# Kernel optimization log

Measured on AMD Instinct MI355X. Metric: run time of the kernel, lower is better.

Reference implementation:

```python
import jax, jax.numpy as jnp
import numpy as np

D_K = 64
NEG_INF = -1.0e9

def setup_inputs() -> dict:
    key = jax.random.key(0)
    kq, kk, kv, km = jax.random.split(key, 4)
    B, H, S, D = 2, 16, 2048, D_K
    Q = jax.random.normal(kq, (B, H, S, D), dtype=jnp.float32)
    K = jax.random.normal(kk, (B, H, S, D), dtype=jnp.float32)
    V = jax.random.normal(kv, (B, H, S, D), dtype=jnp.float32)
    # True entries are masked out (torch masked_fill semantics)
    attn_mask = jax.random.randint(km, (B, H, S, S), 0, 2).astype(jnp.bool_)
    return {"Q": Q, "K": K, "V": V, "attn_mask": attn_mask}

def reference(Q, K, V, attn_mask):
    # scores: [B, H, len_q, len_k]
    scale = 1.0 / np.sqrt(D_K).astype(np.float32)
    scores = jnp.einsum('bhqd,bhkd->bhqk', Q, K) * scale
    scores = jnp.where(attn_mask, jnp.float32(NEG_INF), scores)
    attn = jax.nn.softmax(scores, axis=-1)
    prob = jnp.einsum('bhqk,bhkd->bhqd', attn, V)
    return (prob, attn)
```

## Files before the change

### kernel.cpp

```cpp
#include <hip/hip_runtime.h>
#include <hip/hip_bf16.h>

#define S_LEN 2048
#define D_DIM 64
#define QT    64
#define KT    64
#define NTHR  256
#define NKT   (S_LEN / KT)
#define NBLK  1024
#define PROB_ELEMS 4194304LL

typedef float        f32x4  __attribute__((ext_vector_type(4)));
typedef int          i32x4  __attribute__((ext_vector_type(4)));
typedef unsigned int u32x4  __attribute__((ext_vector_type(4)));
typedef short        bf16x8 __attribute__((ext_vector_type(8)));

__device__ __forceinline__ unsigned short f2bf(float f) {
    return __builtin_bit_cast(unsigned short, __float2bfloat16(f));
}
__device__ __forceinline__ int swzc(int row, int ch) {
    return ch ^ ((row ^ (row >> 3)) & 7);
}
__device__ __forceinline__ float4 scale4(float4 v, float s) {
    v.x *= s; v.y *= s; v.z *= s; v.w *= s; return v;
}
__device__ __forceinline__ u32x4 packbf(float4 a, float4 b) {
    u32x4 r;
    r[0] = (unsigned)f2bf(a.x) | ((unsigned)f2bf(a.y) << 16);
    r[1] = (unsigned)f2bf(a.z) | ((unsigned)f2bf(a.w) << 16);
    r[2] = (unsigned)f2bf(b.x) | ((unsigned)f2bf(b.y) << 16);
    r[3] = (unsigned)f2bf(b.z) | ((unsigned)f2bf(b.w) << 16);
    return r;
}
__device__ __forceinline__ unsigned cvtpk(float lo, float hi) {
    unsigned r;
    asm("v_cvt_pk_bf16_f32 %0, %1, %2" : "=v"(r) : "v"(lo), "v"(hi));
    return r;
}
__device__ __forceinline__ void glds16(const unsigned* g, unsigned char* l) {
    __builtin_amdgcn_global_load_lds(
        (const __attribute__((address_space(1))) unsigned*)g,
        (__attribute__((address_space(3))) unsigned*)(void*)l, 16, 0, 0);
}

__global__ void mask_probe_kernel(const unsigned int* __restrict__ m,
                                  int* __restrict__ flag) {
    unsigned int v = m[threadIdx.x];
    unsigned long long ok = __ballot(v <= 1u);
    if (threadIdx.x == 0) *flag = (ok == ~0ULL) ? 1 : 0;
}

#define KPART 524288
#define VPART 65536
__global__ __launch_bounds__(256)
void kv_prep(const float* __restrict__ Kg, const float* __restrict__ Vg,
             unsigned* __restrict__ Kbf, unsigned* __restrict__ Vtb) {
    int tid = blockIdx.x * 256 + threadIdx.x;
    if (tid < KPART) {
        int ch = tid & 7, rowg = tid >> 3;
        const float* src = Kg + (long long)rowg * D_DIM + ch * 8;
        float4 a = *(const float4*)src, b = *(const float4*)(src + 4);
        int bh = rowg >> 11, k = rowg & 2047, kt = k >> 6, row = k & 63;
        unsigned* dst = Kbf + ((unsigned)(bh * NKT + kt) << 11)
                            + row * 32 + swzc(row, ch) * 4;
        *(u32x4*)dst = packbf(a, b);
    } else if (tid < KPART + VPART) {
        int idx = tid - KPART;
        int d = idx & 63, kt = (idx >> 6) & 31, bh = idx >> 11;
        const float* vb = Vg + (long long)(bh * S_LEN + kt * KT) * D_DIM + d;
        unsigned* tile = Vtb + ((unsigned)(bh * NKT + kt) << 11) + d * 32;
        #pragma unroll
        for (int ci = 0; ci < 8; ++ci) {
            u32x4 o;
            #pragma unroll
            for (int s = 0; s < 4; ++s) {
                float lo = vb[(ci * 8 + 2 * s) * D_DIM];
                float hi = vb[(ci * 8 + 2 * s + 1) * D_DIM];
                o[s] = (unsigned)f2bf(lo) | ((unsigned)f2bf(hi) << 16);
            }
            *(u32x4*)(tile + swzc(d, ci) * 4) = o;
        }
    }
}


#define LOAD_MBITS(DST, KTV)                                                \
    { unsigned bz = 0u;                                                     \
      _Pragma("unroll")                                                     \
      for (int n = 0; n < 4; ++n) {                                         \
        unsigned idx = rowoff + (unsigned)((KTV) * KT + n * 16 + 4 * g);    \
        if (mask32) {                                                       \
            i32x4 m4 = *(const i32x4*)(((const int*)maskB) + idx);          \
            bz |= ((m4[0] ? 1u : 0u) | (m4[1] ? 2u : 0u) |                  \
                   (m4[2] ? 4u : 0u) | (m4[3] ? 8u : 0u)) << (n * 4);       \
        } else {                                                            \
            unsigned mb = *(const unsigned*)(maskB + idx);                  \
            bz |= (((mb & 0xffu) ? 1u : 0u) | ((mb & 0xff00u) ? 2u : 0u) |  \
                   ((mb & 0xff0000u) ? 4u : 0u) |                           \
                   ((mb & 0xff000000u) ? 8u : 0u)) << (n * 4);              \
        } }                                                                 \
      (DST) = bz; }

#define LOAD_BITS2(DST, KTV)                                                \
    { if (useWS) (DST) = (unsigned)bitsWS[bitbase + (unsigned)(KTV) * NTHR];\
      else LOAD_MBITS(DST, KTV) }

#define PH1_TILE(KS, BITS)                                                  \
    { unsigned bb = (BITS);                                                 \
      _Pragma("unroll")                                                     \
      for (int n = 0; n < 4; ++n) {                                         \
        int rowk = n * 16 + c;                                              \
        bf16x8 kf0 = *(const bf16x8*)((KS) + rowk * 128 + swzc(rowk, g) * 16);     \
        bf16x8 kf1 = *(const bf16x8*)((KS) + rowk * 128 + swzc(rowk, 4 + g) * 16); \
        f32x4 acc = {0.f, 0.f, 0.f, 0.f};                                   \
        acc = __builtin_amdgcn_mfma_f32_16x16x32_bf16(kf0, qf0, acc, 0, 0, 0); \
        acc = __builtin_amdgcn_mfma_f32_16x16x32_bf16(kf1, qf1, acc, 0, 0, 0); \
        unsigned mb = bb >> (n * 4);                                        \
        psum += (mb & 1u) ? 0.f : __expf(acc[0]);                           \
        psum += (mb & 2u) ? 0.f : __expf(acc[1]);                           \
        psum += (mb & 4u) ? 0.f : __expf(acc[2]);                           \
        psum += (mb & 8u) ? 0.f : __expf(acc[3]);                           \
      } }

#define PH2_TILE(KS, VT, BITS, KTV)                                         \
    { unsigned bb = (BITS);                                                 \
      _Pragma("unroll")                                                     \
      for (int n = 0; n < 4; ++n) {                                         \
        int rowk = n * 16 + c;                                              \
        bf16x8 kf0 = *(const bf16x8*)((KS) + rowk * 128 + swzc(rowk, g) * 16);     \
        bf16x8 kf1 = *(const bf16x8*)((KS) + rowk * 128 + swzc(rowk, 4 + g) * 16); \
        f32x4 acc = {0.f, 0.f, 0.f, 0.f};                                   \
        acc = __builtin_amdgcn_mfma_f32_16x16x32_bf16(kf0, qf0, acc, 0, 0, 0); \
        acc = __builtin_amdgcn_mfma_f32_16x16x32_bf16(kf1, qf1, acc, 0, 0, 0); \
        unsigned mb = bb >> (n * 4);                                        \
        f32x4 ev;                                                           \
        ev[0] = (mb & 1u) ? 0.f : __expf(acc[0]) * rinv;                    \
        ev[1] = (mb & 2u) ? 0.f : __expf(acc[1]) * rinv;                    \
        ev[2] = (mb & 4u) ? 0.f : __expf(acc[2]) * rinv;                    \
        ev[3] = (mb & 8u) ? 0.f : __expf(acc[3]) * rinv;                    \
        unsigned idx0 = rowoff + (unsigned)((KTV) * KT + n * 16 + 4 * g);   \
        __builtin_nontemporal_store(ev, (f32x4*)(attnOut + idx0));          \
        uint2 pkv; pkv.x = cvtpk(ev[0], ev[1]); pkv.y = cvtpk(ev[2], ev[3]);\
        int kloc = n * 16 + 4 * g;                                          \
        *(uint2*)(Ps + ql * 128 + swzc(ql, kloc >> 3) * 16 + (kloc & 7) * 2) = pkv; \
      }                                                                     \
      { bf16x8 pa0 = *(const bf16x8*)(Ps + ql * 128 + swzc(ql, g) * 16);    \
        bf16x8 pa1 = *(const bf16x8*)(Ps + ql * 128 + swzc(ql, 4 + g) * 16);\
        __builtin_amdgcn_s_setprio(1);                                      \
        _Pragma("unroll")                                                   \
        for (int df = 0; df < 4; ++df) {                                    \
            int d = df * 16 + c;                                            \
            bf16x8 vb0 = *(const bf16x8*)((VT) + d * 128 + swzc(d, g) * 16);     \
            bf16x8 vb1 = *(const bf16x8*)((VT) + d * 128 + swzc(d, 4 + g) * 16); \
            pacc[df] = __builtin_amdgcn_mfma_f32_16x16x32_bf16(pa0, vb0, pacc[df], 0, 0, 0); \
            pacc[df] = __builtin_amdgcn_mfma_f32_16x16x32_bf16(pa1, vb1, pacc[df], 0, 0, 0); \
        }                                                                   \
        __builtin_amdgcn_s_setprio(0); } }

__global__ __launch_bounds__(NTHR, 4)
void attn_fused_glds(const float* __restrict__ Qg,
                     const unsigned* __restrict__ Kbf,
                     const unsigned* __restrict__ Vtb,
                     const unsigned char* __restrict__ maskB,
                     const int* __restrict__ flagp,
                     unsigned short* __restrict__ bitsWS, int useWS,
                     float* __restrict__ attnOut, float* __restrict__ probOut) {
    __shared__ unsigned char sm[40960];
    unsigned char* Ks0 = sm;
    unsigned char* Ks1 = sm + 8192;
    unsigned char* Vt0 = sm + 16384;
    unsigned char* Vt1 = sm + 24576;
    unsigned char* Ps  = sm + 32768;

    const int t = threadIdx.x;
    const int lane = t & 63, w = t >> 6, c = lane & 15, g = lane >> 4;

    const int orig = blockIdx.x;
    const int virt = (orig & 7) * 128 + (orig >> 3);
    const int qt = virt & 31, bh = virt >> 5;
    const int mask32 = *flagp;

    const int qrowbase = bh * S_LEN + qt * QT;
    const int ql = w * 16 + c;
    const unsigned rowoff = (unsigned)(qrowbase + ql) * (unsigned)S_LEN;
    const unsigned bitbase = (unsigned)virt * NKT * NTHR + (unsigned)t;
    const unsigned ktile0 = (unsigned)(bh * NKT) << 11;

    const int f0u = t * 4, f1u = (NTHR + t) * 4;
    const int dst0 = (t & ~63) * 16, dst1 = (NTHR + (t & ~63)) * 16;

    #pragma unroll
    for (int i = 0; i < 2; ++i) {
        int flat = i * NTHR + t, row = flat >> 3, ch = flat & 7;
        const float* src = Qg + (qrowbase + row) * D_DIM + ch * 8;
        float4 a = *(const float4*)src, b = *(const float4*)(src + 4);
        *(u32x4*)(Ps + row * 128 + swzc(row, ch) * 16) =
            packbf(scale4(a, 0.125f), scale4(b, 0.125f));
    }
    __syncthreads();
    bf16x8 qf0 = *(const bf16x8*)(Ps + ql * 128 + swzc(ql, g) * 16);
    bf16x8 qf1 = *(const bf16x8*)(Ps + ql * 128 + swzc(ql, 4 + g) * 16);

    float psum = 0.f;
    unsigned bA, bB;
    {
        const unsigned* kp = Kbf + ktile0;
        glds16(kp + f0u, Ks0 + dst0);
        glds16(kp + f1u, Ks0 + dst1);
    }
    LOAD_MBITS(bA, 0)

    for (int j = 0; j < NKT / 2; ++j) {
        const int ktA = 2 * j, ktB = 2 * j + 1;
        __syncthreads();
        {
            const unsigned* kp = Kbf + ktile0 + (unsigned)ktB * 2048;
            glds16(kp + f0u, Ks1 + dst0);
            glds16(kp + f1u, Ks1 + dst1);
        }
        LOAD_MBITS(bB, ktB)
        PH1_TILE(Ks0, bA)
        if (useWS) bitsWS[bitbase + (unsigned)ktA * NTHR] = (unsigned short)bA;

        __syncthreads();
        if (j + 1 < NKT / 2) {
            const unsigned* kp = Kbf + ktile0 + (unsigned)(ktA + 2) * 2048;
            glds16(kp + f0u, Ks0 + dst0);
            glds16(kp + f1u, Ks0 + dst1);
            LOAD_MBITS(bA, ktA + 2)
        }
        PH1_TILE(Ks1, bB)
        if (useWS) bitsWS[bitbase + (unsigned)ktB * NTHR] = (unsigned short)bB;
    }

    float s = psum;
    s += __shfl_xor(s, 16, 64);
    s += __shfl_xor(s, 32, 64);
    const float rinv = 1.0f / s;

    f32x4 pacc[4];
    #pragma unroll
    for (int d = 0; d < 4; ++d) pacc[d] = (f32x4){0.f, 0.f, 0.f, 0.f};

    {
        const unsigned* kp = Kbf + ktile0;
        const unsigned* vp = Vtb + ktile0;
        glds16(kp + f0u, Ks0 + dst0); glds16(kp + f1u, Ks0 + dst1);
        glds16(vp + f0u, Vt0 + dst0); glds16(vp + f1u, Vt0 + dst1);
    }
    LOAD_BITS2(bA, 0)

    for (int j = 0; j < NKT / 2; ++j) {
        const int ktA = 2 * j, ktB = 2 * j + 1;
        __syncthreads();
        {
            const unsigned* kp = Kbf + ktile0 + (unsigned)ktB * 2048;
            const unsigned* vp = Vtb + ktile0 + (unsigned)ktB * 2048;
            glds16(kp + f0u, Ks1 + dst0); glds16(kp + f1u, Ks1 + dst1);
            glds16(vp + f0u, Vt1 + dst0); glds16(vp + f1u, Vt1 + dst1);
        }
        LOAD_BITS2(bB, ktB)
        PH2_TILE(Ks0, Vt0, bA, ktA)

        __syncthreads();
        if (j + 1 < NKT / 2) {
            const unsigned* kp = Kbf + ktile0 + (unsigned)(ktA + 2) * 2048;
            const unsigned* vp = Vtb + ktile0 + (unsigned)(ktA + 2) * 2048;
            glds16(kp + f0u, Ks0 + dst0); glds16(kp + f1u, Ks0 + dst1);
            glds16(vp + f0u, Vt0 + dst0); glds16(vp + f1u, Vt0 + dst1);
            LOAD_BITS2(bA, ktA + 2)
        }
        PH2_TILE(Ks1, Vt1, bB, ktB)
    }

    #pragma unroll
    for (int df = 0; df < 4; ++df)
        #pragma unroll
        for (int r = 0; r < 4; ++r) {
            int qe = w * 16 + g * 4 + r;
            probOut[(long long)(qrowbase + qe) * D_DIM + df * 16 + c] = pacc[df][r];
        }
}

#define LOAD_K(KP, KTV)                                                     \
    { _Pragma("unroll")                                                     \
      for (int i = 0; i < 2; ++i) {                                         \
        int flat = i * NTHR + t, row = flat >> 3, ch = flat & 7;            \
        const float* src = Kg + (kbase + (KTV) * KT + row) * D_DIM + ch * 8;\
        float4 a = *(const float4*)src, b = *(const float4*)(src + 4);      \
        KP[i] = packbf(a, b);                                               \
      } }
#define STAGE_K(KS, KP)                                                     \
    { _Pragma("unroll")                                                     \
      for (int i = 0; i < 2; ++i) {                                         \
        int flat = i * NTHR + t, row = flat >> 3, ch = flat & 7;            \
        *(u32x4*)((KS) + row * 128 + swzc(row, ch) * 16) = KP[i];           \
      } }
#define LOAD_V(VP, KTV)                                                     \
    { const float* src = Vg + (kbase + (KTV) * KT + k0v) * D_DIM + dgv * 8; \
      float4 a = *(const float4*)src, b = *(const float4*)(src + 4);        \
      float4 e4 = *(const float4*)(src + D_DIM);                            \
      float4 f4 = *(const float4*)(src + D_DIM + 4);                        \
      VP[0] = (unsigned)f2bf(a.x) | ((unsigned)f2bf(e4.x) << 16);           \
      VP[1] = (unsigned)f2bf(a.y) | ((unsigned)f2bf(e4.y) << 16);           \
      VP[2] = (unsigned)f2bf(a.z) | ((unsigned)f2bf(e4.z) << 16);           \
      VP[3] = (unsigned)f2bf(a.w) | ((unsigned)f2bf(e4.w) << 16);           \
      VP[4] = (unsigned)f2bf(b.x) | ((unsigned)f2bf(f4.x) << 16);           \
      VP[5] = (unsigned)f2bf(b.y) | ((unsigned)f2bf(f4.y) << 16);           \
      VP[6] = (unsigned)f2bf(b.z) | ((unsigned)f2bf(f4.z) << 16);           \
      VP[7] = (unsigned)f2bf(b.w) | ((unsigned)f2bf(f4.w) << 16); }
#define STAGE_V(VT, VP)                                                     \
    { _Pragma("unroll")                                                     \
      for (int jj = 0; jj < 8; ++jj) {                                      \
        int d = dgv * 8 + jj;                                               \
        *(unsigned*)((VT) + d * 128 + swzc(d, k0v >> 3) * 16 + (k0v & 7) * 2) = VP[jj]; \
      } }

__global__ __launch_bounds__(NTHR, 4)
void attn_fused_reg(const float* __restrict__ Qg, const float* __restrict__ Kg,
                    const float* __restrict__ Vg,
                    const unsigned char* __restrict__ maskB,
                    const int* __restrict__ flagp,
                    unsigned short* __restrict__ bitsWS, int useWS,
                    float* __restrict__ attnOut, float* __restrict__ probOut) {
    __shared__ unsigned char sm[40960];
    unsigned char* Ks0 = sm;
    unsigned char* Ks1 = sm + 8192;
    unsigned char* Vt0 = sm + 16384;
    unsigned char* Vt1 = sm + 24576;
    unsigned char* Ps  = sm + 32768;

    const int t = threadIdx.x;
    const int lane = t & 63, w = t >> 6, c = lane & 15, g = lane >> 4;

    const int orig = blockIdx.x;
    const int virt = (orig & 7) * 128 + (orig >> 3);
    const int qt = virt & 31, bh = virt >> 5;
    const int mask32 = *flagp;

    const int qrowbase = bh * S_LEN + qt * QT;
    const int kbase = bh * S_LEN;
    const int ql = w * 16 + c;
    const unsigned rowoff = (unsigned)(qrowbase + ql) * (unsigned)S_LEN;
    const unsigned bitbase = (unsigned)virt * NKT * NTHR + (unsigned)t;
    const int dgv = t & 7, k0v = (t >> 3) * 2;

    #pragma unroll
    for (int i = 0; i < 2; ++i) {
        int flat = i * NTHR + t, row = flat >> 3, ch = flat & 7;
        const float* src = Qg + (qrowbase + row) * D_DIM + ch * 8;
        float4 a = *(const float4*)src, b = *(const float4*)(src + 4);
        *(u32x4*)(Ps + row * 128 + swzc(row, ch) * 16) =
            packbf(scale4(a, 0.125f), scale4(b, 0.125f));
    }
    __syncthreads();
    bf16x8 qf0 = *(const bf16x8*)(Ps + ql * 128 + swzc(ql, g) * 16);
    bf16x8 qf1 = *(const bf16x8*)(Ps + ql * 128 + swzc(ql, 4 + g) * 16);
    __syncthreads();

    float psum = 0.f;
    u32x4 kpA[2], kpB[2];
    unsigned bA, bB;
    LOAD_K(kpA, 0)
    LOAD_MBITS(bA, 0)

    for (int j = 0; j < NKT / 2; ++j) {
        const int ktA = 2 * j, ktB = 2 * j + 1;
        STAGE_K(Ks0, kpA)
        LOAD_K(kpB, ktB)
        LOAD_MBITS(bB, ktB)
        __syncthreads();
        PH1_TILE(Ks0, bA)
        if (useWS) bitsWS[bitbase + (unsigned)ktA * NTHR] = (unsigned short)bA;
        STAGE_K(Ks1, kpB)
        if (j + 1 < NKT / 2) {
            LOAD_K(kpA, ktA + 2)
            LOAD_MBITS(bA, ktA + 2)
        }
        __syncthreads();
        PH1_TILE(Ks1, bB)
        if (useWS) bitsWS[bitbase + (unsigned)ktB * NTHR] = (unsigned short)bB;
    }

    float s = psum;
    s += __shfl_xor(s, 16, 64);
    s += __shfl_xor(s, 32, 64);
    const float rinv = 1.0f / s;

    f32x4 pacc[4];
    #pragma unroll
    for (int d = 0; d < 4; ++d) pacc[d] = (f32x4){0.f, 0.f, 0.f, 0.f};

    unsigned vpA[8], vpB[8];
    LOAD_K(kpA, 0)
    LOAD_V(vpA, 0)
    LOAD_BITS2(bA, 0)
    __syncthreads();

    for (int j = 0; j < NKT / 2; ++j) {
        const int ktA = 2 * j, ktB = 2 * j + 1;
        STAGE_K(Ks0, kpA)
        STAGE_V(Vt0, vpA)
        LOAD_K(kpB, ktB)
        LOAD_V(vpB, ktB)
        LOAD_BITS2(bB, ktB)
        __syncthreads();
        PH2_TILE(Ks0, Vt0, bA, ktA)
        STAGE_K(Ks1, kpB)
        STAGE_V(Vt1, vpB)
        if (j + 1 < NKT / 2) {
            LOAD_K(kpA, ktA + 2)
            LOAD_V(vpA, ktA + 2)
            LOAD_BITS2(bA, ktA + 2)
        }
        __syncthreads();
        PH2_TILE(Ks1, Vt1, bB, ktB)
    }

    #pragma unroll
    for (int df = 0; df < 4; ++df)
        #pragma unroll
        for (int r = 0; r < 4; ++r) {
            int qe = w * 16 + g * 4 + r;
            probOut[(long long)(qrowbase + qe) * D_DIM + df * 16 + c] = pacc[df][r];
        }
}

extern "C" void kernel_launch(void* const* d_in, const int* in_sizes, int n_in,
                              void* d_out, int out_size, void* d_ws, size_t ws_size,
                              hipStream_t stream) {
    const float* Q = (const float*)d_in[0];
    const float* K = (const float*)d_in[1];
    const float* V = (const float*)d_in[2];
    const unsigned char* mask = (const unsigned char*)d_in[3];

    float* prob = (float*)d_out;
    float* attn = (float*)d_out + PROB_ELEMS;

    const size_t bits_bytes = (size_t)NBLK * NKT * NTHR * 2ull;
    const size_t kbf_bytes  = 8388608ull;
    int* flag = (int*)d_ws;
    unsigned short* bitsWS = (unsigned short*)((char*)d_ws + 256);
    unsigned* Kbf = (unsigned*)((char*)d_ws + 256 + bits_bytes);
    unsigned* Vtb = (unsigned*)((char*)d_ws + 256 + bits_bytes + kbf_bytes);

    const int useWS   = (ws_size >= 256 + bits_bytes) ? 1 : 0;
    const int usePrep = (ws_size >= 256 + bits_bytes + 2 * kbf_bytes) ? 1 : 0;

    mask_probe_kernel<<<1, 64, 0, stream>>>((const unsigned int*)mask, flag);
    if (usePrep) {
        kv_prep<<<(KPART + VPART) / 256, 256, 0, stream>>>(K, V, Kbf, Vtb);
        attn_fused_glds<<<NBLK, NTHR, 0, stream>>>(Q, Kbf, Vtb, mask, flag,
                                                   bitsWS, useWS, attn, prob);
    } else {
        attn_fused_reg<<<NBLK, NTHR, 0, stream>>>(Q, K, V, mask, flag,
                                                  bitsWS, useWS, attn, prob);
    }
}
```

Baseline: 365.3 us.

## Split key range across waves with MFMA-fragment K/V layout loaded directly to registers

Replaces the LDS-staged global_load_lds kernel with a new kernel that uses 32-row query tiles and splits each 64-key tile between two waves. K and V are pre-packed into per-lane MFMA fragment order, so each wave loads its operands straight from global memory into registers, with no LDS staging and no per-tile barriers. Row sums and the partial P·V accumulators are combined across the two wave halves through shared memory, and the mask bit cache shrinks to 8-bit entries. The block count doubles and occupancy is hinted at 4 blocks per CU. In exchange it adds a cross-wave reduction and relies on L2 to serve K/V reads that LDS used to share.

Measured after the change: 441.5 us. +20.9%, slower.

```diff
diff --git a/kernel.cpp b/kernel.cpp
--- a/kernel.cpp
+++ b/kernel.cpp
@@ -3,11 +3,12 @@
 
 #define S_LEN 2048
 #define D_DIM 64
-#define QT    64
+#define QT    32
 #define KT    64
 #define NTHR  256
 #define NKT   (S_LEN / KT)
-#define NBLK  1024
+#define NQT   (S_LEN / QT)
+#define NBLK  (NQT * 32)
 #define PROB_ELEMS 4194304LL
 
 typedef float        f32x4  __attribute__((ext_vector_type(4)));
@@ -37,11 +38,8 @@
     asm("v_cvt_pk_bf16_f32 %0, %1, %2" : "=v"(r) : "v"(lo), "v"(hi));
     return r;
 }
-__device__ __forceinline__ void glds16(const unsigned* g, unsigned char* l) {
-    __builtin_amdgcn_global_load_lds(
-        (const __attribute__((address_space(1))) unsigned*)g,
-        (__attribute__((address_space(3))) unsigned*)(void*)l, 16, 0, 0);
-}
+#define BC8(x) __builtin_bit_cast(bf16x8, (x))
+#define MFMA(A, B, C) __builtin_amdgcn_mfma_f32_16x16x32_bf16((A), (B), (C), 0, 0, 0)
 
 __global__ void mask_probe_kernel(const unsigned int* __restrict__ m,
                                   int* __restrict__ flag) {
@@ -50,59 +48,278 @@
     if (threadIdx.x == 0) *flag = (ok == ~0ULL) ? 1 : 0;
 }
 
-#define KPART 524288
-#define VPART 65536
+#define KFRAG_T 524288
+#define VFRAG_T 524288
 __global__ __launch_bounds__(256)
-void kv_prep(const float* __restrict__ Kg, const float* __restrict__ Vg,
-             unsigned* __restrict__ Kbf, unsigned* __restrict__ Vtb) {
+void kv_prep_split(const float* __restrict__ Kg, const float* __restrict__ Vg,
+                   unsigned* __restrict__ Kf, unsigned* __restrict__ Vf) {
     int tid = blockIdx.x * 256 + threadIdx.x;
-    if (tid < KPART) {
-        int ch = tid & 7, rowg = tid >> 3;
-        const float* src = Kg + (long long)rowg * D_DIM + ch * 8;
+    if (tid < KFRAG_T) {
+        int l = tid & 63, f = (tid >> 6) & 1, n = (tid >> 7) & 1;
+        int wk = (tid >> 8) & 1, kt = (tid >> 9) & 31, bh = tid >> 14;
+        int c = l & 15, g = l >> 4;
+        const float* src = Kg
+            + (long long)(bh * S_LEN + kt * KT + wk * 32 + n * 16 + c) * D_DIM
+            + f * 32 + g * 8;
         float4 a = *(const float4*)src, b = *(const float4*)(src + 4);
-        int bh = rowg >> 11, k = rowg & 2047, kt = k >> 6, row = k & 63;
-        unsigned* dst = Kbf + ((unsigned)(bh * NKT + kt) << 11)
-                            + row * 32 + swzc(row, ch) * 4;
+        unsigned* dst = Kf + ((unsigned)(bh * NKT + kt) << 11)
+                           + (unsigned)((wk * 4 + n * 2 + f) * 64 + l) * 4u;
         *(u32x4*)dst = packbf(a, b);
-    } else if (tid < KPART + VPART) {
-        int idx = tid - KPART;
-        int d = idx & 63, kt = (idx >> 6) & 31, bh = idx >> 11;
-        const float* vb = Vg + (long long)(bh * S_LEN + kt * KT) * D_DIM + d;
-        unsigned* tile = Vtb + ((unsigned)(bh * NKT + kt) << 11) + d * 32;
+    } else if (tid < KFRAG_T + VFRAG_T) {
+        int idx = tid - KFRAG_T;
+        int l = idx & 63, df = (idx >> 6) & 3;
+        int wk = (idx >> 8) & 1, kt = (idx >> 9) & 31, bh = idx >> 14;
+        int c = l & 15, g = l >> 4;
+        const float* vb = Vg
+            + (long long)(bh * S_LEN + kt * KT + wk * 32 + g * 8) * D_DIM
+            + df * 16 + c;
+        u32x4 o;
         #pragma unroll
-        for (int ci = 0; ci < 8; ++ci) {
-            u32x4 o;
+        for (int s = 0; s < 4; ++s) {
+            float lo = vb[(2 * s) * D_DIM];
+            float hi = vb[(2 * s + 1) * D_DIM];
+            o[s] = (unsigned)f2bf(lo) | ((unsigned)f2bf(hi) << 16);
+        }
+        unsigned* dst = Vf + ((unsigned)(bh * NKT + kt) << 11)
+                           + (unsigned)((wk * 4 + df) * 64 + l) * 4u;
+        *(u32x4*)dst = o;
+    }
+}
+
+#define LOAD_KF(DST, KTV)                                                   \
+    { const u32x4* p_ = (const u32x4*)(Kf + tbase + (unsigned)(KTV) * 2048u \
+                                       + (unsigned)wk * 1024u) + lane;      \
+      DST[0] = p_[0]; DST[1] = p_[64]; DST[2] = p_[128]; DST[3] = p_[192]; }
+
+#define LOAD_VF(DST, KTV)                                                   \
+    { const u32x4* p_ = (const u32x4*)(Vf + tbase + (unsigned)(KTV) * 2048u \
+                                       + (unsigned)wk * 1024u) + lane;      \
+      DST[0] = p_[0]; DST[1] = p_[64]; DST[2] = p_[128]; DST[3] = p_[192]; }
+
+#define PREF_MSK(M4, R2, KTV)                                               \
+    { if (mask32) {                                                         \
+        _Pragma("unroll")                                                   \
+        for (int n_ = 0; n_ < 2; ++n_)                                      \
+          M4[n_] = *(const i32x4*)(maskI + rowoff                           \
+                     + (unsigned)((KTV) * KT + wk * 32 + n_ * 16 + 4 * g)); \
+      } else {                                                              \
+        _Pragma("unroll")                                                   \
+        for (int n_ = 0; n_ < 2; ++n_)                                      \
+          R2[n_] = *(const unsigned*)(maskB + rowoff                        \
+                     + (unsigned)((KTV) * KT + wk * 32 + n_ * 16 + 4 * g)); \
+      } }
+
+#define BITS8(DST, M4, R2)                                                  \
+    { unsigned bz_ = 0u;                                                    \
+      if (mask32) {                                                         \
+        _Pragma("unroll")                                                   \
+        for (int n_ = 0; n_ < 2; ++n_)                                      \
+          bz_ |= ((M4[n_][0] ? 1u : 0u) | (M4[n_][1] ? 2u : 0u) |           \
+                  (M4[n_][2] ? 4u : 0u) | (M4[n_][3] ? 8u : 0u)) << (n_*4); \
+      } else {                                                              \
+        _Pragma("unroll")                                                   \
+        for (int n_ = 0; n_ < 2; ++n_) { unsigned mb_ = R2[n_];             \
+          bz_ |= (((mb_ & 0xffu) ? 1u : 0u) | ((mb_ & 0xff00u) ? 2u : 0u) | \
+                  ((mb_ & 0xff0000u) ? 4u : 0u) |                           \
+                  ((mb_ & 0xff000000u) ? 8u : 0u)) << (n_ * 4); }           \
+      }                                                                     \
+      (DST) = bz_; }
+
+#define LOAD_B8(DST, KTV)                                                   \
+    { if (useWS) (DST) = (unsigned)bitsWS[bitbase + (unsigned)(KTV)*NTHR];  \
+      else { i32x4 mq_[2]; unsigned rq_[2];                                 \
+             PREF_MSK(mq_, rq_, KTV) BITS8(DST, mq_, rq_) } }
+
+#define QK4(KC, A0, A1)                                                     \
+    { A0 = (f32x4){0.f,0.f,0.f,0.f}; A1 = (f32x4){0.f,0.f,0.f,0.f};         \
+      A0 = MFMA(BC8(KC[0]), qf0, A0); A0 = MFMA(BC8(KC[1]), qf1, A0);       \
+      A1 = MFMA(BC8(KC[2]), qf0, A1); A1 = MFMA(BC8(KC[3]), qf1, A1); }
+
+#define PH1(KC, BITS)                                                       \
+    { f32x4 a0_, a1_; QK4(KC, a0_, a1_)                                     \
+      unsigned bb_ = (BITS);                                                \
+      psum += (bb_ &   1u) ? 0.f : __expf(a0_[0]);                          \
+      psum += (bb_ &   2u) ? 0.f : __expf(a0_[1]);                          \
+      psum += (bb_ &   4u) ? 0.f : __expf(a0_[2]);                          \
+      psum += (bb_ &   8u) ? 0.f : __expf(a0_[3]);                          \
+      psum += (bb_ &  16u) ? 0.f : __expf(a1_[0]);                          \
+      psum += (bb_ &  32u) ? 0.f : __expf(a1_[1]);                          \
+      psum += (bb_ &  64u) ? 0.f : __expf(a1_[2]);                          \
+      psum += (bb_ & 128u) ? 0.f : __expf(a1_[3]); }
+
+#define PH2(KC, VC, BITS, KTV)                                              \
+    { f32x4 a0_, a1_; QK4(KC, a0_, a1_)                                     \
+      unsigned bb_ = (BITS);                                                \
+      f32x4 e0_, e1_;                                                       \
+      e0_[0] = (bb_ &   1u) ? 0.f : __expf(a0_[0]) * rinv;                  \
+      e0_[1] = (bb_ &   2u) ? 0.f : __expf(a0_[1]) * rinv;                  \
+      e0_[2] = (bb_ &   4u) ? 0.f : __expf(a0_[2]) * rinv;                  \
+      e0_[3] = (bb_ &   8u) ? 0.f : __expf(a0_[3]) * rinv;                  \
+      e1_[0] = (bb_ &  16u) ? 0.f : __expf(a1_[0]) * rinv;                  \
+      e1_[1] = (bb_ &  32u) ? 0.f : __expf(a1_[1]) * rinv;                  \
+      e1_[2] = (bb_ &  64u) ? 0.f : __expf(a1_[2]) * rinv;                  \
+      e1_[3] = (bb_ & 128u) ? 0.f : __expf(a1_[3]) * rinv;                  \
+      unsigned ix_ = rowoff + (unsigned)((KTV) * KT + wk * 32 + 4 * g);     \
+      *(f32x4*)(attnOut + ix_)      = e0_;                                  \
+      *(f32x4*)(attnOut + ix_ + 16) = e1_;                                  \
+      { uint2 p0_, p1_;                                                     \
+        p0_.x = cvtpk(e0_[0], e0_[1]); p0_.y = cvtpk(e0_[2], e0_[3]);       \
+        p1_.x = cvtpk(e1_[0], e1_[1]); p1_.y = cvtpk(e1_[2], e1_[3]);       \
+        *(uint2*)(PsW + c * 80 + 8 * g)      = p0_;                         \
+        *(uint2*)(PsW + c * 80 + 32 + 8 * g) = p1_; }                       \
+      { bf16x8 pa_ = *(const bf16x8*)(PsW + c * 80 + 16 * g);               \
+        __builtin_amdgcn_s_setprio(1);                                      \
+        pacc[0] = MFMA(pa_, BC8(VC[0]), pacc[0]);                           \
+        pacc[1] = MFMA(pa_, BC8(VC[1]), pacc[1]);                           \
+        pacc[2] = MFMA(pa_, BC8(VC[2]), pacc[2]);                           \
+        pacc[3] = MFMA(pa_, BC8(VC[3]), pacc[3]);                           \
+        __builtin_amdgcn_s_setprio(0); } }
+
+#define QS_OFF 0
+#define PS_OFF 4096
+#define RS_OFF 9216
+#define SMB    9472
+
+__global__ __launch_bounds__(NTHR, 4)
+void attn_fused_split(const float* __restrict__ Qg,
+                      const unsigned* __restrict__ Kf,
+                      const unsigned* __restrict__ Vf,
+                      const unsigned char* __restrict__ maskB,
+                      const int* __restrict__ flagp,
+                      unsigned char* __restrict__ bitsWS, int useWS,
+                      float* __restrict__ attnOut, float* __restrict__ probOut) {
+    __shared__ unsigned char sm[SMB];
+
+    const int t = threadIdx.x;
+    const int lane = t & 63, w = t >> 6, c = lane & 15, g = lane >> 4;
+    const int wq = w >> 1, wk = w & 1;
+
+    const int orig = blockIdx.x;
+    const int virt = (orig & 7) * 256 + (orig >> 3);
+    const int qt = virt & (NQT - 1), bh = virt >> 6;
+    const int mask32 = *flagp;
+    const int* maskI = (const int*)maskB;
+
+    const int qrowbase = bh * S_LEN + qt * QT;
+    const unsigned rowoff = (unsigned)(qrowbase + wq * 16 + c) * (unsigned)S_LEN;
+    const unsigned bitbase = (unsigned)virt * NKT * NTHR + (unsigned)t;
+    const unsigned tbase = (unsigned)(bh * NKT) << 11;
+    unsigned char* PsW = sm + PS_OFF + w * 1280;
+
+    {
+        int row = t >> 3, ch = t & 7;
+        const float* src = Qg + (qrowbase + row) * D_DIM + ch * 8;
+        float4 a = *(const float4*)src, b = *(const float4*)(src + 4);
+        *(u32x4*)(sm + QS_OFF + row * 128 + swzc(row, ch) * 16) =
+            packbf(scale4(a, 0.125f), scale4(b, 0.125f));
+    }
+    __syncthreads();
+    bf16x8 qf0, qf1;
+    {
+        int row = wq * 16 + c;
+        qf0 = *(const bf16x8*)(sm + QS_OFF + row * 128 + swzc(row, g) * 16);
+        qf1 = *(const bf16x8*)(sm + QS_OFF + row * 128 + swzc(row, 4 + g) * 16);
+    }
+
+    float psum = 0.f;
+    {
+        u32x4 kA[4], kB[4];
+        i32x4 mA[2], mB[2];
+        unsigned rA[2], rB[2], bA, bB;
+        LOAD_KF(kA, 0)
+        PREF_MSK(mA, rA, 0)
+        for (int j = 0; j < NKT / 2; ++j) {
+            const int ktA = 2 * j, ktB = 2 * j + 1;
+            LOAD_KF(kB, ktB)
+            PREF_MSK(mB, rB, ktB)
+            BITS8(bA, mA, rA)
+            PH1(kA, bA)
+            if (useWS) bitsWS[bitbase + (unsigned)ktA * NTHR] = (unsigned char)bA;
+            if (j + 1 < NKT / 2) {
+                LOAD_KF(kA, ktA + 2)
+                PREF_MSK(mA, rA, ktA + 2)
+            }
+            BITS8(bB, mB, rB)
+            PH1(kB, bB)
+            if (useWS) bitsWS[bitbase + (unsigned)ktB * NTHR] = (unsigned char)bB;
+        }
+    }
+    {
+        float s = psum;
+        s += __shfl_xor(s, 16, 64);
+        s += __shfl_xor(s, 32, 64);
+        float* Rs = (float*)(sm + RS_OFF);
+        if (lane < 16) Rs[w * 16 + c] = s;
+    }
+    __syncthreads();
+    const float rinv = 1.0f /
+        (((const float*)(sm + RS_OFF))[(wq * 2 + 0) * 16 + c] +
+         ((const float*)(sm + RS_OFF))[(wq * 2 + 1) * 16 + c]);
+
+    f32x4 pacc[4];
+    #pragma unroll
+    for (int d = 0; d < 4; ++d) pacc[d] = (f32x4){0.f, 0.f, 0.f, 0.f};
+    {
+        u32x4 kA[4], kB[4], vA[4], vB[4];
+        unsigned bA, bB;
+        LOAD_KF(kA, 0)
+        LOAD_B8(bA, 0)
+        for (int j = 0; j < NKT / 2; ++j) {
+            const int ktA = 2 * j, ktB = 2 * j + 1;
+            LOAD_KF(kB, ktB)
+            LOAD_B8(bB, ktB)
+            LOAD_VF(vA, ktA)
+            PH2(kA, vA, bA, ktA)
+            if (j + 1 < NKT / 2) {
+                LOAD_KF(kA, ktA + 2)
+                LOAD_B8(bA, ktA + 2)
+            }
+            LOAD_VF(vB, ktB)
+            PH2(kB, vB, bB, ktB)
+        }
+    }
+
+    __syncthreads();
+    if (wk == 1) {
+        #pragma unroll
+        for (int df = 0; df < 4; ++df)
+            *(f32x4*)(sm + wq * 4096 + lane * 64 + df * 16) = pacc[df];
+    }
+    __syncthreads();
+    if (wk == 0) {
+        #pragma unroll
+        for (int df = 0; df < 4; ++df) {
+            f32x4 o = pacc[df] +
+                *(const f32x4*)(sm + wq * 4096 + lane * 64 + df * 16);
             #pragma unroll
-            for (int s = 0; s < 4; ++s) {
-                float lo = vb[(ci * 8 + 2 * s) * D_DIM];
-                float hi = vb[(ci * 8 + 2 * s + 1) * D_DIM];
-                o[s] = (unsigned)f2bf(lo) | ((unsigned)f2bf(hi) << 16);
+            for (int r = 0; r < 4; ++r) {
+                int qe = qrowbase + wq * 16 + 4 * g + r;
+                probOut[(long long)qe * D_DIM + df * 16 + c] = o[r];
             }
-            *(u32x4*)(tile + swzc(d, ci) * 4) = o;
-        }
-    }
-}
-
-
+        }
+    }
+}
+
+#define FKT 64
 #define LOAD_MBITS(DST, KTV)                                                \
-    { unsigned bz = 0u;                                                     \
+    { unsigned bz_ = 0u;                                                    \
       _Pragma("unroll")                                                     \
-      for (int n = 0; n < 4; ++n) {                                         \
-        unsigned idx = rowoff + (unsigned)((KTV) * KT + n * 16 + 4 * g);    \
+      for (int n_ = 0; n_ < 4; ++n_) {                                      \
+        unsigned idx_ = rowoff + (unsigned)((KTV) * FKT + n_ * 16 + 4 * g); \
         if (mask32) {                                                       \
-            i32x4 m4 = *(const i32x4*)(((const int*)maskB) + idx);          \
-            bz |= ((m4[0] ? 1u : 0u) | (m4[1] ? 2u : 0u) |                  \
-                   (m4[2] ? 4u : 0u) | (m4[3] ? 8u : 0u)) << (n * 4);       \
+            i32x4 m4_ = *(const i32x4*)(maskI + idx_);                      \
+            bz_ |= ((m4_[0] ? 1u : 0u) | (m4_[1] ? 2u : 0u) |               \
+                    (m4_[2] ? 4u : 0u) | (m4_[3] ? 8u : 0u)) << (n_ * 4);   \
         } else {                                                            \
-            unsigned mb = *(const unsigned*)(maskB + idx);                  \
-            bz |= (((mb & 0xffu) ? 1u : 0u) | ((mb & 0xff00u) ? 2u : 0u) |  \
-                   ((mb & 0xff0000u) ? 4u : 0u) |                           \
-                   ((mb & 0xff000000u) ? 8u : 0u)) << (n * 4);              \
+            unsigned mb_ = *(const unsigned*)(maskB + idx_);                \
+            bz_ |= (((mb_ & 0xffu) ? 1u : 0u) | ((mb_ & 0xff00u) ? 2u : 0u) | \
+                    ((mb_ & 0xff0000u) ? 4u : 0u) |                         \
+                    ((mb_ & 0xff000000u) ? 8u : 0u)) << (n_ * 4);           \
         } }                                                                 \
-      (DST) = bz; }
+      (DST) = bz_; }
 
 #define LOAD_BITS2(DST, KTV)                                                \
-    { if (useWS) (DST) = (unsigned)bitsWS[bitbase + (unsigned)(KTV) * NTHR];\
+    { if (useWS) (DST) = (unsigned)bitsW16[bitbase + (unsigned)(KTV)*NTHR]; \
       else LOAD_MBITS(DST, KTV) }
 
 #define PH1_TILE(KS, BITS)                                                  \
@@ -113,8 +330,7 @@
         bf16x8 kf0 = *(const bf16x8*)((KS) + rowk * 128 + swzc(rowk, g) * 16);     \
         bf16x8 kf1 = *(const bf16x8*)((KS) + rowk * 128 + swzc(rowk, 4 + g) * 16); \
         f32x4 acc = {0.f, 0.f, 0.f, 0.f};                                   \
-        acc = __builtin_amdgcn_mfma_f32_16x16x32_bf16(kf0, qf0, acc, 0, 0, 0); \
-        acc = __builtin_amdgcn_mfma_f32_16x16x32_bf16(kf1, qf1, acc, 0, 0, 0); \
+        acc = MFMA(kf0, qf0, acc); acc = MFMA(kf1, qf1, acc);               \
         unsigned mb = bb >> (n * 4);                                        \
         psum += (mb & 1u) ? 0.f : __expf(acc[0]);                           \
         psum += (mb & 2u) ? 0.f : __expf(acc[1]);                           \
@@ -130,163 +346,35 @@
         bf16x8 kf0 = *(const bf16x8*)((KS) + rowk * 128 + swzc(rowk, g) * 16);     \
         bf16x8 kf1 = *(const bf16x8*)((KS) + rowk * 128 + swzc(rowk, 4 + g) * 16); \
         f32x4 acc = {0.f, 0.f, 0.f, 0.f};                                   \
-        acc = __builtin_amdgcn_mfma_f32_16x16x32_bf16(kf0, qf0, acc, 0, 0, 0); \
-        acc = __builtin_amdgcn_mfma_f32_16x16x32_bf16(kf1, qf1, acc, 0, 0, 0); \
+        acc = MFMA(kf0, qf0, acc); acc = MFMA(kf1, qf1, acc);               \
         unsigned mb = bb >> (n * 4);                                        \
         f32x4 ev;                                                           \
         ev[0] = (mb & 1u) ? 0.f : __expf(acc[0]) * rinv;                    \
         ev[1] = (mb & 2u) ? 0.f : __expf(acc[1]) * rinv;                    \
         ev[2] = (mb & 4u) ? 0.f : __expf(acc[2]) * rinv;                    \
         ev[3] = (mb & 8u) ? 0.f : __expf(acc[3]) * rinv;                    \
-        unsigned idx0 = rowoff + (unsigned)((KTV) * KT + n * 16 + 4 * g);   \
-        __builtin_nontemporal_store(ev, (f32x4*)(attnOut + idx0));          \
+        unsigned idx0 = rowoff + (unsigned)((KTV) * FKT + n * 16 + 4 * g);  \
+        *(f32x4*)(attnOut + idx0) = ev;                                     \
         uint2 pkv; pkv.x = cvtpk(ev[0], ev[1]); pkv.y = cvtpk(ev[2], ev[3]);\
         int kloc = n * 16 + 4 * g;                                          \
         *(uint2*)(Ps + ql * 128 + swzc(ql, kloc >> 3) * 16 + (kloc & 7) * 2) = pkv; \
       }                                                                     \
       { bf16x8 pa0 = *(const bf16x8*)(Ps + ql * 128 + swzc(ql, g) * 16);    \
         bf16x8 pa1 = *(const bf16x8*)(Ps + ql * 128 + swzc(ql, 4 + g) * 16);\
-        __builtin_amdgcn_s_setprio(1);                                      \
         _Pragma("unroll")                                                   \
         for (int df = 0; df < 4; ++df) {                                    \
             int d = df * 16 + c;                                            \
             bf16x8 vb0 = *(const bf16x8*)((VT) + d * 128 + swzc(d, g) * 16);     \
             bf16x8 vb1 = *(const bf16x8*)((VT) + d * 128 + swzc(d, 4 + g) * 16); \
-            pacc[df] = __builtin_amdgcn_mfma_f32_16x16x32_bf16(pa0, vb0, pacc[df], 0, 0, 0); \
-            pacc[df] = __builtin_amdgcn_mfma_f32_16x16x32_bf16(pa1, vb1, pacc[df], 0, 0, 0); \
-        }                                                                   \
-        __builtin_amdgcn_s_setprio(0); } }
-
-__global__ __launch_bounds__(NTHR, 4)
-void attn_fused_glds(const float* __restrict__ Qg,
-                     const unsigned* __restrict__ Kbf,
-                     const unsigned* __restrict__ Vtb,
-                     const unsigned char* __restrict__ maskB,
-                     const int* __restrict__ flagp,
-                     unsigned short* __restrict__ bitsWS, int useWS,
-                     float* __restrict__ attnOut, float* __restrict__ probOut) {
-    __shared__ unsigned char sm[40960];
-    unsigned char* Ks0 = sm;
-    unsigned char* Ks1 = sm + 8192;
-    unsigned char* Vt0 = sm + 16384;
-    unsigned char* Vt1 = sm + 24576;
-    unsigned char* Ps  = sm + 32768;
-
-    const int t = threadIdx.x;
-    const int lane = t & 63, w = t >> 6, c = lane & 15, g = lane >> 4;
-
-    const int orig = blockIdx.x;
-    const int virt = (orig & 7) * 128 + (orig >> 3);
-    const int qt = virt & 31, bh = virt >> 5;
-    const int mask32 = *flagp;
-
-    const int qrowbase = bh * S_LEN + qt * QT;
-    const int ql = w * 16 + c;
-    const unsigned rowoff = (unsigned)(qrowbase + ql) * (unsigned)S_LEN;
-    const unsigned bitbase = (unsigned)virt * NKT * NTHR + (unsigned)t;
-    const unsigned ktile0 = (unsigned)(bh * NKT) << 11;
-
-    const int f0u = t * 4, f1u = (NTHR + t) * 4;
-    const int dst0 = (t & ~63) * 16, dst1 = (NTHR + (t & ~63)) * 16;
-
-    #pragma unroll
-    for (int i = 0; i < 2; ++i) {
-        int flat = i * NTHR + t, row = flat >> 3, ch = flat & 7;
-        const float* src = Qg + (qrowbase + row) * D_DIM + ch * 8;
-        float4 a = *(const float4*)src, b = *(const float4*)(src + 4);
-        *(u32x4*)(Ps + row * 128 + swzc(row, ch) * 16) =
-            packbf(scale4(a, 0.125f), scale4(b, 0.125f));
-    }
-    __syncthreads();
-    bf16x8 qf0 = *(const bf16x8*)(Ps + ql * 128 + swzc(ql, g) * 16);
-    bf16x8 qf1 = *(const bf16x8*)(Ps + ql * 128 + swzc(ql, 4 + g) * 16);
-
-    float psum = 0.f;
-    unsigned bA, bB;
-    {
-        const unsigned* kp = Kbf + ktile0;
-        glds16(kp + f0u, Ks0 + dst0);
-        glds16(kp + f1u, Ks0 + dst1);
-    }
-    LOAD_MBITS(bA, 0)
-
-    for (int j = 0; j < NKT / 2; ++j) {
-        const int ktA = 2 * j, ktB = 2 * j + 1;
-        __syncthreads();
-        {
-            const unsigned* kp = Kbf + ktile0 + (unsigned)ktB * 2048;
-            glds16(kp + f0u, Ks1 + dst0);
-            glds16(kp + f1u, Ks1 + dst1);
-        }
-        LOAD_MBITS(bB, ktB)
-        PH1_TILE(Ks0, bA)
-        if (useWS) bitsWS[bitbase + (unsigned)ktA * NTHR] = (unsigned short)bA;
-
-        __syncthreads();
-        if (j + 1 < NKT / 2) {
-            const unsigned* kp = Kbf + ktile0 + (unsigned)(ktA + 2) * 2048;
-            glds16(kp + f0u, Ks0 + dst0);
-            glds16(kp + f1u, Ks0 + dst1);
-            LOAD_MBITS(bA, ktA + 2)
-        }
-        PH1_TILE(Ks1, bB)
-        if (useWS) bitsWS[bitbase + (unsigned)ktB * NTHR] = (unsigned short)bB;
-    }
-
-    float s = psum;
-    s += __shfl_xor(s, 16, 64);
-    s += __shfl_xor(s, 32, 64);
-    const float rinv = 1.0f / s;
-
-    f32x4 pacc[4];
-    #pragma unroll
-    for (int d = 0; d < 4; ++d) pacc[d] = (f32x4){0.f, 0.f, 0.f, 0.f};
-
-    {
-        const unsigned* kp = Kbf + ktile0;
-        const unsigned* vp = Vtb + ktile0;
-        glds16(kp + f0u, Ks0 + dst0); glds16(kp + f1u, Ks0 + dst1);
-        glds16(vp + f0u, Vt0 + dst0); glds16(vp + f1u, Vt0 + dst1);
-    }
-    LOAD_BITS2(bA, 0)
-
-    for (int j = 0; j < NKT / 2; ++j) {
-        const int ktA = 2 * j, ktB = 2 * j + 1;
-        __syncthreads();
-        {
-            const unsigned* kp = Kbf + ktile0 + (unsigned)ktB * 2048;
-            const unsigned* vp = Vtb + ktile0 + (unsigned)ktB * 2048;
-            glds16(kp + f0u, Ks1 + dst0); glds16(kp + f1u, Ks1 + dst1);
-            glds16(vp + f0u, Vt1 + dst0); glds16(vp + f1u, Vt1 + dst1);
-        }
-        LOAD_BITS2(bB, ktB)
-        PH2_TILE(Ks0, Vt0, bA, ktA)
-
-        __syncthreads();
-        if (j + 1 < NKT / 2) {
-            const unsigned* kp = Kbf + ktile0 + (unsigned)(ktA + 2) * 2048;
-            const unsigned* vp = Vtb + ktile0 + (unsigned)(ktA + 2) * 2048;
-            glds16(kp + f0u, Ks0 + dst0); glds16(kp + f1u, Ks0 + dst1);
-            glds16(vp + f0u, Vt0 + dst0); glds16(vp + f1u, Vt0 + dst1);
-            LOAD_BITS2(bA, ktA + 2)
-        }
-        PH2_TILE(Ks1, Vt1, bB, ktB)
-    }
-
-    #pragma unroll
-    for (int df = 0; df < 4; ++df)
-        #pragma unroll
-        for (int r = 0; r < 4; ++r) {
-            int qe = w * 16 + g * 4 + r;
-            probOut[(long long)(qrowbase + qe) * D_DIM + df * 16 + c] = pacc[df][r];
-        }
-}
+            pacc[df] = MFMA(pa0, vb0, pacc[df]);                            \
+            pacc[df] = MFMA(pa1, vb1, pacc[df]);                            \
+        } } }
 
 #define LOAD_K(KP, KTV)                                                     \
     { _Pragma("unroll")                                                     \
       for (int i = 0; i < 2; ++i) {                                         \
         int flat = i * NTHR + t, row = flat >> 3, ch = flat & 7;            \
-        const float* src = Kg + (kbase + (KTV) * KT + row) * D_DIM + ch * 8;\
+        const float* src = Kg + (kbase + (KTV) * FKT + row) * D_DIM + ch*8; \
         float4 a = *(const float4*)src, b = *(const float4*)(src + 4);      \
         KP[i] = packbf(a, b);                                               \
       } }
@@ -297,7 +385,7 @@
         *(u32x4*)((KS) + row * 128 + swzc(row, ch) * 16) = KP[i];           \
       } }
 #define LOAD_V(VP, KTV)                                                     \
-    { const float* src = Vg + (kbase + (KTV) * KT + k0v) * D_DIM + dgv * 8; \
+    { const float* src = Vg + (kbase + (KTV) * FKT + k0v) * D_DIM + dgv*8;  \
       float4 a = *(const float4*)src, b = *(const float4*)(src + 4);        \
       float4 e4 = *(const float4*)(src + D_DIM);                            \
       float4 f4 = *(const float4*)(src + D_DIM + 4);                        \
@@ -321,7 +409,7 @@
                     const float* __restrict__ Vg,
                     const unsigned char* __restrict__ maskB,
                     const int* __restrict__ flagp,
-                    unsigned short* __restrict__ bitsWS, int useWS,
+                    unsigned short* __restrict__ bitsW16, int useWS,
                     float* __restrict__ attnOut, float* __restrict__ probOut) {
     __shared__ unsigned char sm[40960];
     unsigned char* Ks0 = sm;
@@ -332,13 +420,15 @@
 
     const int t = threadIdx.x;
     const int lane = t & 63, w = t >> 6, c = lane & 15, g = lane >> 4;
+    (void)lane;
 
     const int orig = blockIdx.x;
     const int virt = (orig & 7) * 128 + (orig >> 3);
     const int qt = virt & 31, bh = virt >> 5;
     const int mask32 = *flagp;
-
-    const int qrowbase = bh * S_LEN + qt * QT;
+    const int* maskI = (const int*)maskB;
+
+    const int qrowbase = bh * S_LEN + qt * 64;
     const int kbase = bh * S_LEN;
     const int ql = w * 16 + c;
     const unsigned rowoff = (unsigned)(qrowbase + ql) * (unsigned)S_LEN;
@@ -371,7 +461,7 @@
         LOAD_MBITS(bB, ktB)
         __syncthreads();
         PH1_TILE(Ks0, bA)
-        if (useWS) bitsWS[bitbase + (unsigned)ktA * NTHR] = (unsigned short)bA;
+        if (useWS) bitsW16[bitbase + (unsigned)ktA * NTHR] = (unsigned short)bA;
         STAGE_K(Ks1, kpB)
         if (j + 1 < NKT / 2) {
             LOAD_K(kpA, ktA + 2)
@@ -379,7 +469,7 @@
         }
         __syncthreads();
         PH1_TILE(Ks1, bB)
-        if (useWS) bitsWS[bitbase + (unsigned)ktB * NTHR] = (unsigned short)bB;
+        if (useWS) bitsW16[bitbase + (unsigned)ktB * NTHR] = (unsigned short)bB;
     }
 
     float s = psum;
@@ -437,23 +527,24 @@
     float* prob = (float*)d_out;
     float* attn = (float*)d_out + PROB_ELEMS;
 
-    const size_t bits_bytes = (size_t)NBLK * NKT * NTHR * 2ull;
+    const size_t bits_bytes = 16777216ull;
     const size_t kbf_bytes  = 8388608ull;
     int* flag = (int*)d_ws;
-    unsigned short* bitsWS = (unsigned short*)((char*)d_ws + 256);
-    unsigned* Kbf = (unsigned*)((char*)d_ws + 256 + bits_bytes);
-    unsigned* Vtb = (unsigned*)((char*)d_ws + 256 + bits_bytes + kbf_bytes);
+    unsigned char*  bits8  = (unsigned char*)((char*)d_ws + 256);
+    unsigned short* bits16 = (unsigned short*)((char*)d_ws + 256);
+    unsigned* Kf = (unsigned*)((char*)d_ws + 256 + bits_bytes);
+    unsigned* Vf = (unsigned*)((char*)d_ws + 256 + bits_bytes + kbf_bytes);
 
     const int useWS   = (ws_size >= 256 + bits_bytes) ? 1 : 0;
     const int usePrep = (ws_size >= 256 + bits_bytes + 2 * kbf_bytes) ? 1 : 0;
 
     mask_probe_kernel<<<1, 64, 0, stream>>>((const unsigned int*)mask, flag);
     if (usePrep) {
-        kv_prep<<<(KPART + VPART) / 256, 256, 0, stream>>>(K, V, Kbf, Vtb);
-        attn_fused_glds<<<NBLK, NTHR, 0, stream>>>(Q, Kbf, Vtb, mask, flag,
-                                                   bitsWS, useWS, attn, prob);
+        kv_prep_split<<<(KFRAG_T + VFRAG_T) / 256, 256, 0, stream>>>(K, V, Kf, Vf);
+        attn_fused_split<<<NBLK, NTHR, 0, stream>>>(Q, Kf, Vf, mask, flag,
+                                                    bits8, useWS, attn, prob);
     } else {
-        attn_fused_reg<<<NBLK, NTHR, 0, stream>>>(Q, K, V, mask, flag,
-                                                  bitsWS, useWS, attn, prob);
-    }
-}
+        attn_fused_reg<<<1024, NTHR, 0, stream>>>(Q, K, V, mask, flag,
+                                                  bits16, useWS, attn, prob);
+    }
+}
```
